# Optimization experiments

Measured on AMD Instinct MI355X. Metric: run time of the kernel, lower is better.

The kernel has to match this reference:

```python
import jax, jax.numpy as jnp
import numpy as np

N_NODES = 100000


def _gcn_layer(h, W, b, src, dst, norm, n):
    # h: [N, Fin] -> transform then normalized scatter-add aggregation
    h = h @ W                                   # [N, Fout]
    msg = h[src] * norm[:, None]                # [E', Fout] gather + scale
    out = jax.ops.segment_sum(msg, dst, num_segments=n)  # scatter-add
    return out + b


def setup_inputs() -> dict:
    key = jax.random.key(0)
    k1, k2, k3, k4 = jax.random.split(key, 4)
    N, F_IN, HID, C, E = N_NODES, 512, 128, 40, 1600000
    x = jax.random.normal(k1, (N, F_IN), dtype=jnp.float32)
    edge_index = jax.random.randint(k2, (2, E), 0, N, dtype=jnp.int64)
    W1 = jax.random.normal(k3, (F_IN, HID), dtype=jnp.float32) * (1.0 / np.sqrt(F_IN))
    b1 = jnp.zeros((HID,), dtype=jnp.float32)
    W2 = jax.random.normal(k4, (HID, C), dtype=jnp.float32) * (1.0 / np.sqrt(HID))
    b2 = jnp.zeros((C,), dtype=jnp.float32)
    return {"x": x, "edge_index": edge_index, "W1": W1, "b1": b1, "W2": W2, "b2": b2}


def reference(x, edge_index, W1, b1, W2, b2):
    n = x.shape[0]
    # add self-loops (GCNConv default)
    loop = jnp.arange(n, dtype=edge_index.dtype)
    src = jnp.concatenate([edge_index[0], loop])
    dst = jnp.concatenate([edge_index[1], loop])
    # symmetric normalization: deg counted on destination (in-degree, incl. self-loop)
    deg = jax.ops.segment_sum(jnp.ones_like(dst, dtype=x.dtype), dst, num_segments=n)
    dis = jnp.where(deg > 0, jax.lax.rsqrt(deg), 0.0)  # deg^{-1/2}
    norm = dis[src] * dis[dst]                          # per-edge weight

    h = jax.nn.relu(_gcn_layer(x, W1, b1, src, dst, norm, n))
    # dropout: identity in eval mode (training=False)
    h = _gcn_layer(h, W2, b2, src, dst, norm, n)
    return jax.nn.log_softmax(h, axis=1)
```

## Files before the change

### kernel.cpp

```cpp
#include <hip/hip_runtime.h>
#include <hip/hip_bf16.h>


#define F_IN 512
#define HID  128
#define NC   40

typedef __attribute__((ext_vector_type(8))) short bf16x8;
typedef __attribute__((ext_vector_type(4))) float f32x4v;

__device__ __forceinline__ ushort f2bf(float f) {
    union { float f; unsigned u; } x; x.f = f;
    unsigned r = x.u + 0x7FFFu + ((x.u >> 16) & 1u);
    return (ushort)(r >> 16);
}
__device__ __forceinline__ float bf2f(ushort u) {
    return __uint_as_float((unsigned)u << 16);
}

__global__ void count_deg(const int* __restrict__ dst, int E, unsigned* __restrict__ cnt) {
    int t = blockIdx.x * blockDim.x + threadIdx.x;
    if (t < E) atomicAdd(&cnt[dst[t]], 1u);
}

__global__ __launch_bounds__(1024) void scan_block(const unsigned* __restrict__ cnt,
                                                   unsigned* __restrict__ offs,
                                                   unsigned* __restrict__ bsums,
                                                   float* __restrict__ dis, int N) {
    __shared__ unsigned s[1024];
    int tid = threadIdx.x;
    int i = blockIdx.x * 1024 + tid;
    unsigned v = (i < N) ? cnt[i] : 0u;
    if (i < N) dis[i] = rsqrtf((float)v + 1.0f);
    s[tid] = v;
    __syncthreads();
    #pragma unroll
    for (int d = 1; d < 1024; d <<= 1) {
        unsigned t = (tid >= d) ? s[tid - d] : 0u;
        __syncthreads();
        s[tid] += t;
        __syncthreads();
    }
    if (i < N) offs[i] = s[tid] - v;
    if (tid == 1023) bsums[blockIdx.x] = s[1023];
}

__global__ __launch_bounds__(1024) void scan_bsums(unsigned* __restrict__ bsums, int nb) {
    __shared__ unsigned s[1024];
    int tid = threadIdx.x;
    unsigned v = (tid < nb) ? bsums[tid] : 0u;
    s[tid] = v;
    __syncthreads();
    #pragma unroll
    for (int d = 1; d < 1024; d <<= 1) {
        unsigned t = (tid >= d) ? s[tid - d] : 0u;
        __syncthreads();
        s[tid] += t;
        __syncthreads();
    }
    if (tid < nb) bsums[tid] = s[tid] - v;
}

__global__ __launch_bounds__(1024) void scan_add(unsigned* __restrict__ offs,
                                                 const unsigned* __restrict__ bsums,
                                                 int N, unsigned total) {
    int i = blockIdx.x * 1024 + threadIdx.x;
    if (i < N) offs[i] += bsums[blockIdx.x];
    if (i == 0) offs[N] = total;
}

__global__ void fill_csr(const int* __restrict__ src, const int* __restrict__ dst,
                         const unsigned* __restrict__ offs, unsigned* __restrict__ cursor,
                         int* __restrict__ col, int E) {
    int t = blockIdx.x * blockDim.x + threadIdx.x;
    if (t >= E) return;
    int s = src[t], d = dst[t];
    unsigned pos = offs[d] + atomicAdd(&cursor[d], 1u);
    col[pos] = s;
}

__global__ void packW(const float* __restrict__ W1, const float* __restrict__ W2,
                      ushort* __restrict__ W1p, ushort* __restrict__ W2p) {
    int t = blockIdx.x * 256 + threadIdx.x;
    if (t < 65536) {
        int j = t & 7, n = (t >> 3) & 127, kb = (t >> 10) & 3, s = t >> 12;
        int k = s * 32 + kb * 8 + j;
        W1p[t] = f2bf(W1[(size_t)k * HID + n]);
    } else {
        int q = t - 65536;
        if (q < 6144) {
            int j = q & 7;
            int i2 = q >> 3;
            int n = i2 % 48;
            int i3 = i2 / 48;
            int kb = i3 & 3, ks = i3 >> 2;
            int k = ks * 32 + kb * 8 + j;
            float v = (n < NC) ? W2[(size_t)k * NC + n] : 0.f;
            W2p[q] = f2bf(v);
        }
    }
}

__global__ __launch_bounds__(256) void gemm1_mfma(const float* __restrict__ A,
                                                  const ushort* __restrict__ Bp,
                                                  const float* __restrict__ dis,
                                                  ushort* __restrict__ C, int N) {
    __shared__ __align__(16) ushort Bs[2][4096];
    const int tid  = threadIdx.x;
    const int wave = tid >> 6;
    const int lane = tid & 63;
    const int quad = lane >> 4;
    const int mr   = lane & 15;
    const int bm   = blockIdx.x * 128;

    const int r0 = bm + wave * 32 + mr;
    const int r1 = r0 + 16;
    const bool ok0 = r0 < N, ok1 = r1 < N;
    const float* arow0 = A + (size_t)r0 * F_IN + quad * 8;
    const float* arow1 = A + (size_t)r1 * F_IN + quad * 8;

    f32x4v acc[2][8];
    #pragma unroll
    for (int i = 0; i < 2; i++)
        #pragma unroll
        for (int t = 0; t < 8; t++)
            acc[i][t] = (f32x4v){0.f, 0.f, 0.f, 0.f};

    {
        const uint4* sp = (const uint4*)Bp;
        uint4* dp = (uint4*)Bs[0];
        dp[tid] = sp[tid];
        dp[tid + 256] = sp[tid + 256];
    }
    __syncthreads();

    for (int s = 0; s < 16; s++) {
        if (s < 15) {
            const uint4* sp = (const uint4*)(Bp + (size_t)(s + 1) * 4096);
            uint4* dp = (uint4*)Bs[(s + 1) & 1];
            dp[tid] = sp[tid];
            dp[tid + 256] = sp[tid + 256];
        }
        float4 z = make_float4(0.f, 0.f, 0.f, 0.f);
        float4 a0l = ok0 ? *(const float4*)(arow0 + s * 32)     : z;
        float4 a0h = ok0 ? *(const float4*)(arow0 + s * 32 + 4) : z;
        float4 a1l = ok1 ? *(const float4*)(arow1 + s * 32)     : z;
        float4 a1h = ok1 ? *(const float4*)(arow1 + s * 32 + 4) : z;
        __align__(16) ushort ta[8], tb[8];
        ta[0]=f2bf(a0l.x); ta[1]=f2bf(a0l.y); ta[2]=f2bf(a0l.z); ta[3]=f2bf(a0l.w);
        ta[4]=f2bf(a0h.x); ta[5]=f2bf(a0h.y); ta[6]=f2bf(a0h.z); ta[7]=f2bf(a0h.w);
        tb[0]=f2bf(a1l.x); tb[1]=f2bf(a1l.y); tb[2]=f2bf(a1l.z); tb[3]=f2bf(a1l.w);
        tb[4]=f2bf(a1h.x); tb[5]=f2bf(a1h.y); tb[6]=f2bf(a1h.z); tb[7]=f2bf(a1h.w);
        bf16x8 fa0 = *(const bf16x8*)ta;
        bf16x8 fa1 = *(const bf16x8*)tb;
        const ushort* bbase = Bs[s & 1] + quad * 1024;
        #pragma unroll
        for (int t = 0; t < 8; t++) {
            bf16x8 b = *(const bf16x8*)&bbase[(t * 16 + mr) * 8];
            acc[0][t] = __builtin_amdgcn_mfma_f32_16x16x32_bf16(fa0, b, acc[0][t], 0, 0, 0);
            acc[1][t] = __builtin_amdgcn_mfma_f32_16x16x32_bf16(fa1, b, acc[1][t], 0, 0, 0);
        }
        __syncthreads();
    }
    #pragma unroll
    for (int i = 0; i < 2; i++) {
        int row0 = bm + wave * 32 + i * 16 + quad * 4;
        #pragma unroll
        for (int rr = 0; rr < 4; rr++) {
            int row = row0 + rr;
            if (row < N) {
                float ds = dis[row];
                #pragma unroll
                for (int t = 0; t < 8; t++)
                    C[(size_t)row * HID + t * 16 + mr] = f2bf(acc[i][t][rr] * ds);
            }
        }
    }
}

__global__ __launch_bounds__(256) void agg1_k(const ushort* __restrict__ h,
                                              const int* __restrict__ col,
                                              const unsigned* __restrict__ offs,
                                              const float* __restrict__ dis,
                                              ushort* __restrict__ out, int N) {
    int node = blockIdx.x * 16 + (threadIdx.x >> 4);
    if (node >= N) return;
    int lane = threadIdx.x & 15;
    const size_t coff = (size_t)lane * 8;
    float a0[8], a1[8] = {}, a2[8] = {}, a3[8] = {};
    {
        uint4 v = *(const uint4*)(h + (size_t)node * HID + coff);
        const ushort* u = (const ushort*)&v;
        #pragma unroll
        for (int j = 0; j < 8; j++) a0[j] = bf2f(u[j]);
    }
    unsigned p0 = offs[node], p1 = offs[node + 1];
    unsigned p = p0;
    for (; p + 4 <= p1; p += 4) {
        int s0 = col[p], s1 = col[p+1], s2 = col[p+2], s3 = col[p+3];
        uint4 v0 = *(const uint4*)(h + (size_t)s0 * HID + coff);
        uint4 v1 = *(const uint4*)(h + (size_t)s1 * HID + coff);
        uint4 v2 = *(const uint4*)(h + (size_t)s2 * HID + coff);
        uint4 v3 = *(const uint4*)(h + (size_t)s3 * HID + coff);
        const ushort* u0 = (const ushort*)&v0;
        const ushort* u1 = (const ushort*)&v1;
        const ushort* u2 = (const ushort*)&v2;
        const ushort* u3 = (const ushort*)&v3;
        #pragma unroll
        for (int j = 0; j < 8; j++) {
            a0[j] += bf2f(u0[j]); a1[j] += bf2f(u1[j]);
            a2[j] += bf2f(u2[j]); a3[j] += bf2f(u3[j]);
        }
    }
    for (; p < p1; ++p) {
        int s = col[p];
        uint4 v = *(const uint4*)(h + (size_t)s * HID + coff);
        const ushort* u = (const ushort*)&v;
        #pragma unroll
        for (int j = 0; j < 8; j++) a0[j] += bf2f(u[j]);
    }
    float dd = dis[node];
    __align__(16) ushort o[8];
    #pragma unroll
    for (int j = 0; j < 8; j++)
        o[j] = f2bf(((a0[j] + a1[j]) + (a2[j] + a3[j])) * dd);
    *(uint4*)(out + (size_t)node * HID + coff) = *(const uint4*)o;
}

__global__ __launch_bounds__(256) void gemm2_mfma(const ushort* __restrict__ A,
                                                  const float* __restrict__ b1,
                                                  const ushort* __restrict__ W2p,
                                                  const float* __restrict__ dis,
                                                  ushort* __restrict__ h2, int N) {
    __shared__ __align__(16) ushort As[128 * 136];
    __shared__ __align__(16) ushort Bs[6144];
    const int tid = threadIdx.x;
    const int bm = blockIdx.x * 128;

    {
        const uint4* s4 = (const uint4*)W2p;
        uint4* d4 = (uint4*)Bs;
        #pragma unroll
        for (int i = 0; i < 3; i++) d4[tid + i * 256] = s4[tid + i * 256];
    }
    {
        const int r  = tid >> 1;
        const int hh = tid & 1;
        const int row = bm + r;
        const float* brow = b1 + hh * 64;
        if (row < N) {
            const ushort* arow = A + (size_t)row * HID + hh * 64;
            #pragma unroll
            for (int i = 0; i < 8; i++) {
                uint4 raw = *(const uint4*)(arow + i * 8);
                const ushort* u = (const ushort*)&raw;
                __align__(16) ushort tmp[8];
                #pragma unroll
                for (int j = 0; j < 8; j++)
                    tmp[j] = f2bf(fmaxf(bf2f(u[j]) + brow[i * 8 + j], 0.f));
                *(uint4*)&As[r * 136 + hh * 64 + i * 8] = *(const uint4*)tmp;
            }
        } else {
            #pragma unroll
            for (int i = 0; i < 8; i++) {
                uint4 zz = {0, 0, 0, 0};
                *(uint4*)&As[r * 136 + hh * 64 + i * 8] = zz;
            }
        }
    }
    __syncthreads();

    const int wave = tid >> 6;
    const int lane = tid & 63;
    const int quad = lane >> 4;
    const int mr   = lane & 15;
    f32x4v acc[2][3];
    #pragma unroll
    for (int i = 0; i < 2; i++)
        #pragma unroll
        for (int t = 0; t < 3; t++)
            acc[i][t] = (f32x4v){0.f, 0.f, 0.f, 0.f};
    #pragma unroll
    for (int ks = 0; ks < 4; ks++) {
        bf16x8 a0 = *(const bf16x8*)&As[(wave * 32 + mr) * 136 + ks * 32 + quad * 8];
        bf16x8 a1 = *(const bf16x8*)&As[(wave * 32 + 16 + mr) * 136 + ks * 32 + quad * 8];
        #pragma unroll
        for (int t = 0; t < 3; t++) {
            bf16x8 b = *(const bf16x8*)&Bs[((ks * 4 + quad) * 48 + t * 16 + mr) * 8];
            acc[0][t] = __builtin_amdgcn_mfma_f32_16x16x32_bf16(a0, b, acc[0][t], 0, 0, 0);
            acc[1][t] = __builtin_amdgcn_mfma_f32_16x16x32_bf16(a1, b, acc[1][t], 0, 0, 0);
        }
    }
    #pragma unroll
    for (int i = 0; i < 2; i++) {
        #pragma unroll
        for (int rr = 0; rr < 4; rr++) {
            int node = bm + wave * 32 + i * 16 + quad * 4 + rr;
            if (node < N) {
                float ds = dis[node];
                #pragma unroll
                for (int t = 0; t < 3; t++) {
                    int c = t * 16 + mr;
                    if (c < NC)
                        h2[(size_t)node * NC + c] = f2bf(acc[i][t][rr] * ds);
                }
            }
        }
    }
}

__global__ __launch_bounds__(256) void agg2_ls(const ushort* __restrict__ h2,
                                               const int* __restrict__ col,
                                               const unsigned* __restrict__ offs,
                                               const float* __restrict__ dis,
                                               const float* __restrict__ b2,
                                               float* __restrict__ out, int N) {
    int node = blockIdx.x * 32 + (threadIdx.x >> 3);
    if (node >= N) return;
    int lane = threadIdx.x & 7;
    const bool act = lane < 5;
    const size_t coff = (size_t)lane * 8;
    float a[8] = {}, c[8] = {};
    if (act) {
        uint4 v = *(const uint4*)(h2 + (size_t)node * NC + coff);
        const ushort* u = (const ushort*)&v;
        #pragma unroll
        for (int j = 0; j < 8; j++) a[j] = bf2f(u[j]);
    }
    unsigned p0 = offs[node], p1 = offs[node + 1];
    unsigned p = p0;
    for (; p + 2 <= p1; p += 2) {
        int s0 = col[p], s1 = col[p + 1];
        if (act) {
            uint4 v0 = *(const uint4*)(h2 + (size_t)s0 * NC + coff);
            uint4 v1 = *(const uint4*)(h2 + (size_t)s1 * NC + coff);
            const ushort* u0 = (const ushort*)&v0;
            const ushort* u1 = (const ushort*)&v1;
            #pragma unroll
            for (int j = 0; j < 8; j++) { a[j] += bf2f(u0[j]); c[j] += bf2f(u1[j]); }
        }
    }
    for (; p < p1; ++p) {
        int s = col[p];
        if (act) {
            uint4 v = *(const uint4*)(h2 + (size_t)s * NC + coff);
            const ushort* u = (const ushort*)&v;
            #pragma unroll
            for (int j = 0; j < 8; j++) a[j] += bf2f(u[j]);
        }
    }
    float dd = dis[node];
    float l[8];
    float m = -1e30f;
    if (act) {
        #pragma unroll
        for (int j = 0; j < 8; j++) {
            l[j] = (a[j] + c[j]) * dd + b2[lane * 8 + j];
            m = fmaxf(m, l[j]);
        }
    }
    #pragma unroll
    for (int d = 1; d < 8; d <<= 1) m = fmaxf(m, __shfl_xor(m, d, 8));
    float s = 0.f;
    if (act) {
        #pragma unroll
        for (int j = 0; j < 8; j++) s += __expf(l[j] - m);
    }
    #pragma unroll
    for (int d = 1; d < 8; d <<= 1) s += __shfl_xor(s, d, 8);
    float lse = m + __logf(s);
    if (act) {
        float* op = out + (size_t)node * NC + lane * 8;
        *(float4*)op       = make_float4(l[0]-lse, l[1]-lse, l[2]-lse, l[3]-lse);
        *(float4*)(op + 4) = make_float4(l[4]-lse, l[5]-lse, l[6]-lse, l[7]-lse);
    }
}

extern "C" void kernel_launch(void* const* d_in, const int* in_sizes, int n_in,
                              void* d_out, int out_size, void* d_ws, size_t ws_size,
                              hipStream_t stream) {
    const float* x  = (const float*)d_in[0];
    const int*   ei = (const int*)d_in[1];
    const float* W1 = (const float*)d_in[2];
    const float* b1 = (const float*)d_in[3];
    const float* W2 = (const float*)d_in[4];
    const float* b2 = (const float*)d_in[5];
    float* out = (float*)d_out;

    const int N = in_sizes[0] / F_IN;
    const int E = in_sizes[1] / 2;
    const int* src = ei;
    const int* dst = ei + E;

    char* ws = (char*)d_ws;
    size_t o = 0;
    unsigned* cnt  = (unsigned*)(ws + o); o += (size_t)N * 4;
    unsigned* cur  = (unsigned*)(ws + o); o += (size_t)N * 4;
    float*    dis  = (float*)   (ws + o); o += (size_t)N * 4;
    unsigned* offs = (unsigned*)(ws + o); o += (size_t)(N + 4) * 4;
    unsigned* bsums= (unsigned*)(ws + o); o += 4096;
    int*      col  = (int*)     (ws + o); o += (size_t)E * 4;
    o = (o + 15) & ~(size_t)15;
    ushort*   W1p  = (ushort*)  (ws + o); o += (size_t)F_IN * HID * 2;
    o = (o + 15) & ~(size_t)15;
    ushort*   W2p  = (ushort*)  (ws + o); o += 6144 * 2;
    o = (o + 15) & ~(size_t)15;
    ushort*   h1   = (ushort*)  (ws + o); o += (size_t)N * HID * 2;
    o = (o + 15) & ~(size_t)15;
    ushort*   ag1  = (ushort*)  (ws + o); o += (size_t)N * HID * 2;
    o = (o + 15) & ~(size_t)15;
    ushort*   h2   = (ushort*)  (ws + o); o += (size_t)N * NC * 2;

    const int nb = (N + 1023) / 1024;

    hipMemsetAsync(cnt, 0, (size_t)N * 8, stream);
    count_deg<<<(E + 255) / 256, 256, 0, stream>>>(dst, E, cnt);
    scan_block<<<nb, 1024, 0, stream>>>(cnt, offs, bsums, dis, N);
    scan_bsums<<<1, 1024, 0, stream>>>(bsums, nb);
    scan_add<<<nb, 1024, 0, stream>>>(offs, bsums, N, (unsigned)E);
    fill_csr<<<(E + 255) / 256, 256, 0, stream>>>(src, dst, offs, cur, col, E);

    packW<<<(65536 + 6144 + 255) / 256, 256, 0, stream>>>(W1, W2, W1p, W2p);

    gemm1_mfma<<<(N + 127) / 128, 256, 0, stream>>>(x, W1p, dis, h1, N);
    agg1_k<<<(N + 15) / 16, 256, 0, stream>>>(h1, col, offs, dis, ag1, N);

    gemm2_mfma<<<(N + 127) / 128, 256, 0, stream>>>(ag1, b1, W2p, dis, h2, N);
    agg2_ls<<<(N + 31) / 32, 256, 0, stream>>>(h2, col, offs, dis, b2, out, N);
}
```

Measured before the change: 661.0 us.

## Stage A tiles through LDS with register prefetch, unroll gathers deeper

gemm1 now uses 64-row blocks and loads A cooperatively with coalesced per-thread segments. It converts A to bf16 into a double-buffered LDS tile and prefetches the next A and B slices into registers before the MFMA work, so global latency overlaps compute. The aggregation kernels unroll their neighbor gather loops further (8 rows in agg1, 4 in agg2) with tree sums into a single accumulator to raise memory-level parallelism. The costs are more LDS per block, smaller tiles that reuse B less, and more registers in the gathers.

Result: faster. 636.0 us (-3.8%).

```diff
diff --git a/kernel.cpp b/kernel.cpp
--- a/kernel.cpp
+++ b/kernel.cpp
@@ -105,75 +105,80 @@
                                                   const ushort* __restrict__ Bp,
                                                   const float* __restrict__ dis,
                                                   ushort* __restrict__ C, int N) {
+    __shared__ __align__(16) ushort As[2][64 * 40];
     __shared__ __align__(16) ushort Bs[2][4096];
     const int tid  = threadIdx.x;
     const int wave = tid >> 6;
     const int lane = tid & 63;
     const int quad = lane >> 4;
     const int mr   = lane & 15;
-    const int bm   = blockIdx.x * 128;
-
-    const int r0 = bm + wave * 32 + mr;
-    const int r1 = r0 + 16;
-    const bool ok0 = r0 < N, ok1 = r1 < N;
-    const float* arow0 = A + (size_t)r0 * F_IN + quad * 8;
-    const float* arow1 = A + (size_t)r1 * F_IN + quad * 8;
-
-    f32x4v acc[2][8];
-    #pragma unroll
-    for (int i = 0; i < 2; i++)
-        #pragma unroll
-        for (int t = 0; t < 8; t++)
-            acc[i][t] = (f32x4v){0.f, 0.f, 0.f, 0.f};
-
+    const int bm   = blockIdx.x * 64;
+
+    const int sr = tid >> 2;
+    const int sq = tid & 3;
+    const bool srow_ok = (bm + sr) < N;
+    const float* aptr = A + (size_t)(bm + sr) * F_IN + sq * 8;
+
+    f32x4v acc[8];
+    #pragma unroll
+    for (int t = 0; t < 8; t++) acc[t] = (f32x4v){0.f, 0.f, 0.f, 0.f};
+
+    float4 av0, av1;
+    uint4  bv0, bv1;
+    const float4 z4 = make_float4(0.f, 0.f, 0.f, 0.f);
+
+    av0 = srow_ok ? *(const float4*)(aptr)     : z4;
+    av1 = srow_ok ? *(const float4*)(aptr + 4) : z4;
+    bv0 = ((const uint4*)Bp)[tid];
+    bv1 = ((const uint4*)Bp)[tid + 256];
     {
-        const uint4* sp = (const uint4*)Bp;
-        uint4* dp = (uint4*)Bs[0];
-        dp[tid] = sp[tid];
-        dp[tid + 256] = sp[tid + 256];
+        __align__(16) ushort ta[8];
+        ta[0]=f2bf(av0.x); ta[1]=f2bf(av0.y); ta[2]=f2bf(av0.z); ta[3]=f2bf(av0.w);
+        ta[4]=f2bf(av1.x); ta[5]=f2bf(av1.y); ta[6]=f2bf(av1.z); ta[7]=f2bf(av1.w);
+        *(uint4*)&As[0][sr * 40 + sq * 8] = *(const uint4*)ta;
+        ((uint4*)Bs[0])[tid] = bv0;
+        ((uint4*)Bs[0])[tid + 256] = bv1;
     }
     __syncthreads();
 
     for (int s = 0; s < 16; s++) {
         if (s < 15) {
-            const uint4* sp = (const uint4*)(Bp + (size_t)(s + 1) * 4096);
-            uint4* dp = (uint4*)Bs[(s + 1) & 1];
-            dp[tid] = sp[tid];
-            dp[tid + 256] = sp[tid + 256];
-        }
-        float4 z = make_float4(0.f, 0.f, 0.f, 0.f);
-        float4 a0l = ok0 ? *(const float4*)(arow0 + s * 32)     : z;
-        float4 a0h = ok0 ? *(const float4*)(arow0 + s * 32 + 4) : z;
-        float4 a1l = ok1 ? *(const float4*)(arow1 + s * 32)     : z;
-        float4 a1h = ok1 ? *(const float4*)(arow1 + s * 32 + 4) : z;
-        __align__(16) ushort ta[8], tb[8];
-        ta[0]=f2bf(a0l.x); ta[1]=f2bf(a0l.y); ta[2]=f2bf(a0l.z); ta[3]=f2bf(a0l.w);
-        ta[4]=f2bf(a0h.x); ta[5]=f2bf(a0h.y); ta[6]=f2bf(a0h.z); ta[7]=f2bf(a0h.w);
-        tb[0]=f2bf(a1l.x); tb[1]=f2bf(a1l.y); tb[2]=f2bf(a1l.z); tb[3]=f2bf(a1l.w);
-        tb[4]=f2bf(a1h.x); tb[5]=f2bf(a1h.y); tb[6]=f2bf(a1h.z); tb[7]=f2bf(a1h.w);
-        bf16x8 fa0 = *(const bf16x8*)ta;
-        bf16x8 fa1 = *(const bf16x8*)tb;
-        const ushort* bbase = Bs[s & 1] + quad * 1024;
-        #pragma unroll
-        for (int t = 0; t < 8; t++) {
-            bf16x8 b = *(const bf16x8*)&bbase[(t * 16 + mr) * 8];
-            acc[0][t] = __builtin_amdgcn_mfma_f32_16x16x32_bf16(fa0, b, acc[0][t], 0, 0, 0);
-            acc[1][t] = __builtin_amdgcn_mfma_f32_16x16x32_bf16(fa1, b, acc[1][t], 0, 0, 0);
+            av0 = srow_ok ? *(const float4*)(aptr + (s + 1) * 32)     : z4;
+            av1 = srow_ok ? *(const float4*)(aptr + (s + 1) * 32 + 4) : z4;
+            const uint4* bp = (const uint4*)(Bp + (size_t)(s + 1) * 4096);
+            bv0 = bp[tid];
+            bv1 = bp[tid + 256];
+        }
+        {
+            const ushort* ab = As[s & 1];
+            const ushort* bb = Bs[s & 1] + quad * 1024;
+            bf16x8 a = *(const bf16x8*)&ab[(wave * 16 + mr) * 40 + quad * 8];
+            #pragma unroll
+            for (int t = 0; t < 8; t++) {
+                bf16x8 b = *(const bf16x8*)&bb[(t * 16 + mr) * 8];
+                acc[t] = __builtin_amdgcn_mfma_f32_16x16x32_bf16(a, b, acc[t], 0, 0, 0);
+            }
+        }
+        if (s < 15) {
+            __align__(16) ushort ta[8];
+            ta[0]=f2bf(av0.x); ta[1]=f2bf(av0.y); ta[2]=f2bf(av0.z); ta[3]=f2bf(av0.w);
+            ta[4]=f2bf(av1.x); ta[5]=f2bf(av1.y); ta[6]=f2bf(av1.z); ta[7]=f2bf(av1.w);
+            int nb = (s + 1) & 1;
+            *(uint4*)&As[nb][sr * 40 + sq * 8] = *(const uint4*)ta;
+            ((uint4*)Bs[nb])[tid] = bv0;
+            ((uint4*)Bs[nb])[tid + 256] = bv1;
         }
         __syncthreads();
     }
-    #pragma unroll
-    for (int i = 0; i < 2; i++) {
-        int row0 = bm + wave * 32 + i * 16 + quad * 4;
-        #pragma unroll
-        for (int rr = 0; rr < 4; rr++) {
-            int row = row0 + rr;
-            if (row < N) {
-                float ds = dis[row];
-                #pragma unroll
-                for (int t = 0; t < 8; t++)
-                    C[(size_t)row * HID + t * 16 + mr] = f2bf(acc[i][t][rr] * ds);
-            }
+
+    #pragma unroll
+    for (int rr = 0; rr < 4; rr++) {
+        int row = bm + wave * 16 + quad * 4 + rr;
+        if (row < N) {
+            float ds = dis[row];
+            #pragma unroll
+            for (int t = 0; t < 8; t++)
+                C[(size_t)row * HID + t * 16 + mr] = f2bf(acc[t][rr] * ds);
         }
     }
 }
@@ -187,29 +192,41 @@
     if (node >= N) return;
     int lane = threadIdx.x & 15;
     const size_t coff = (size_t)lane * 8;
-    float a0[8], a1[8] = {}, a2[8] = {}, a3[8] = {};
+    float a[8];
     {
         uint4 v = *(const uint4*)(h + (size_t)node * HID + coff);
         const ushort* u = (const ushort*)&v;
         #pragma unroll
-        for (int j = 0; j < 8; j++) a0[j] = bf2f(u[j]);
+        for (int j = 0; j < 8; j++) a[j] = bf2f(u[j]);
     }
     unsigned p0 = offs[node], p1 = offs[node + 1];
     unsigned p = p0;
-    for (; p + 4 <= p1; p += 4) {
-        int s0 = col[p], s1 = col[p+1], s2 = col[p+2], s3 = col[p+3];
+    for (; p + 8 <= p1; p += 8) {
+        int s0 = col[p],   s1 = col[p+1], s2 = col[p+2], s3 = col[p+3];
+        int s4 = col[p+4], s5 = col[p+5], s6 = col[p+6], s7 = col[p+7];
         uint4 v0 = *(const uint4*)(h + (size_t)s0 * HID + coff);
         uint4 v1 = *(const uint4*)(h + (size_t)s1 * HID + coff);
         uint4 v2 = *(const uint4*)(h + (size_t)s2 * HID + coff);
         uint4 v3 = *(const uint4*)(h + (size_t)s3 * HID + coff);
+        uint4 v4 = *(const uint4*)(h + (size_t)s4 * HID + coff);
+        uint4 v5 = *(const uint4*)(h + (size_t)s5 * HID + coff);
+        uint4 v6 = *(const uint4*)(h + (size_t)s6 * HID + coff);
+        uint4 v7 = *(const uint4*)(h + (size_t)s7 * HID + coff);
         const ushort* u0 = (const ushort*)&v0;
         const ushort* u1 = (const ushort*)&v1;
         const ushort* u2 = (const ushort*)&v2;
         const ushort* u3 = (const ushort*)&v3;
+        const ushort* u4 = (const ushort*)&v4;
+        const ushort* u5 = (const ushort*)&v5;
+        const ushort* u6 = (const ushort*)&v6;
+        const ushort* u7 = (const ushort*)&v7;
         #pragma unroll
         for (int j = 0; j < 8; j++) {
-            a0[j] += bf2f(u0[j]); a1[j] += bf2f(u1[j]);
-            a2[j] += bf2f(u2[j]); a3[j] += bf2f(u3[j]);
+            float t0 = bf2f(u0[j]) + bf2f(u1[j]);
+            float t1 = bf2f(u2[j]) + bf2f(u3[j]);
+            float t2 = bf2f(u4[j]) + bf2f(u5[j]);
+            float t3 = bf2f(u6[j]) + bf2f(u7[j]);
+            a[j] += (t0 + t1) + (t2 + t3);
         }
     }
     for (; p < p1; ++p) {
@@ -217,13 +234,12 @@
         uint4 v = *(const uint4*)(h + (size_t)s * HID + coff);
         const ushort* u = (const ushort*)&v;
         #pragma unroll
-        for (int j = 0; j < 8; j++) a0[j] += bf2f(u[j]);
+        for (int j = 0; j < 8; j++) a[j] += bf2f(u[j]);
     }
     float dd = dis[node];
     __align__(16) ushort o[8];
     #pragma unroll
-    for (int j = 0; j < 8; j++)
-        o[j] = f2bf(((a0[j] + a1[j]) + (a2[j] + a3[j])) * dd);
+    for (int j = 0; j < 8; j++) o[j] = f2bf(a[j] * dd);
     *(uint4*)(out + (size_t)node * HID + coff) = *(const uint4*)o;
 }
 
@@ -320,7 +336,7 @@
     int lane = threadIdx.x & 7;
     const bool act = lane < 5;
     const size_t coff = (size_t)lane * 8;
-    float a[8] = {}, c[8] = {};
+    float a[8] = {};
     if (act) {
         uint4 v = *(const uint4*)(h2 + (size_t)node * NC + coff);
         const ushort* u = (const ushort*)&v;
@@ -329,15 +345,20 @@
     }
     unsigned p0 = offs[node], p1 = offs[node + 1];
     unsigned p = p0;
-    for (; p + 2 <= p1; p += 2) {
-        int s0 = col[p], s1 = col[p + 1];
+    for (; p + 4 <= p1; p += 4) {
+        int s0 = col[p], s1 = col[p + 1], s2 = col[p + 2], s3 = col[p + 3];
         if (act) {
             uint4 v0 = *(const uint4*)(h2 + (size_t)s0 * NC + coff);
             uint4 v1 = *(const uint4*)(h2 + (size_t)s1 * NC + coff);
+            uint4 v2 = *(const uint4*)(h2 + (size_t)s2 * NC + coff);
+            uint4 v3 = *(const uint4*)(h2 + (size_t)s3 * NC + coff);
             const ushort* u0 = (const ushort*)&v0;
             const ushort* u1 = (const ushort*)&v1;
-            #pragma unroll
-            for (int j = 0; j < 8; j++) { a[j] += bf2f(u0[j]); c[j] += bf2f(u1[j]); }
+            const ushort* u2 = (const ushort*)&v2;
+            const ushort* u3 = (const ushort*)&v3;
+            #pragma unroll
+            for (int j = 0; j < 8; j++)
+                a[j] += (bf2f(u0[j]) + bf2f(u1[j])) + (bf2f(u2[j]) + bf2f(u3[j]));
         }
     }
     for (; p < p1; ++p) {
@@ -355,7 +376,7 @@
     if (act) {
         #pragma unroll
         for (int j = 0; j < 8; j++) {
-            l[j] = (a[j] + c[j]) * dd + b2[lane * 8 + j];
+            l[j] = a[j] * dd + b2[lane * 8 + j];
             m = fmaxf(m, l[j]);
         }
     }
@@ -422,7 +443,7 @@
 
     packW<<<(65536 + 6144 + 255) / 256, 256, 0, stream>>>(W1, W2, W1p, W2p);
 
-    gemm1_mfma<<<(N + 127) / 128, 256, 0, stream>>>(x, W1p, dis, h1, N);
+    gemm1_mfma<<<(N + 63) / 64, 256, 0, stream>>>(x, W1p, dis, h1, N);
     agg1_k<<<(N + 15) / 16, 256, 0, stream>>>(h1, col, offs, dis, ag1, N);
 
     gemm2_mfma<<<(N + 127) / 128, 256, 0, stream>>>(ag1, b1, W2p, dis, h2, N);
```
